# Optimization experiments

Measured on AMD Instinct MI355X. Metric: run time of the kernel, lower is better.

Reference implementation:

```python
import jax, jax.numpy as jnp
import numpy as np

# Static config matching init_kwargs
COUT, CIN, K = 64, 64, 3
PAD = K // 2  # padding=1


def setup_inputs() -> dict:
    key = jax.random.key(0)
    k1, k2, k3 = jax.random.split(key, 3)
    B, H, W, FH, FW, SC = 2, 256, 256, 16, 16, 128
    hyper_params = COUT * CIN * K * K  # 36864
    x = jax.random.normal(k1, (B, CIN, H, W), jnp.float32)
    s = jax.random.normal(k2, (B, SC, FH, FW), jnp.float32)
    s2w = jax.random.normal(k3, (hyper_params, SC), jnp.float32) * 0.02
    return {"x": x, "s": s, "s2w": s2w}


def reference(x, s, s2w):
    """HyperPatchConv2d forward: per-patch dynamically generated 3x3 conv.

    x:   [b, c, h, w]   input feature map
    s:   [b, sc, fh, fw] hypernetwork signal (one vector per patch)
    s2w: [P, sc]         signal2weights 1x1 conv (P = out*cin*k*k)
    """
    b, c, h, w = x.shape
    fh, fw = s.shape[-2:]
    ph, pw = h // fh, w // fw          # patch size
    kh, kw = ph + 2 * PAD, pw + 2 * PAD  # unfold window (patch + halo)

    # signal2weights: 1x1 conv -> per-patch flattened conv weight
    wflat = jnp.einsum('pc,bcfg->bfgp', s2w, s)            # [b,fh,fw,P]
    Wdyn = wflat.reshape(b, fh, fw, COUT, CIN, K, K)        # per-patch conv kernels

    # reflect-pad then unfold into overlapping (kh,kw) patches, stride (ph,pw)
    xp = jnp.pad(x, ((0, 0), (0, 0), (PAD, PAD), (PAD, PAD)), mode='reflect')
    idx_h = (jnp.arange(fh) * ph)[:, None] + jnp.arange(kh)[None, :]  # [fh,kh]
    idx_w = (jnp.arange(fw) * pw)[:, None] + jnp.arange(kw)[None, :]  # [fw,kw]
    patches = xp[:, :, idx_h][:, :, :, :, idx_w]            # [b,c,fh,kh,fw,kw]

    # extract KxK sliding windows inside each patch (valid conv, stride 1)
    wi = jnp.arange(ph)[:, None] + jnp.arange(K)[None, :]   # [ph,K]
    wj = jnp.arange(pw)[:, None] + jnp.arange(K)[None, :]   # [pw,K]
    win = patches[:, :, :, wi]                              # [b,c,fh,ph,K,fw,kw]
    win = win[:, :, :, :, :, :, wj]                         # [b,c,fh,ph,K,fw,pw,K]
    win = win.transpose(0, 2, 5, 1, 3, 4, 6, 7)             # [b,fh,fw,c,ph,K,pw,K]

    # per-patch dynamic conv
    out = jnp.einsum('bfgocij,bfgcpiqj->bfgopq', Wdyn, win)  # [b,fh,fw,o,ph,pw]

    # fold: non-overlapping reassembly (stride == patch size)
    return out.transpose(0, 3, 1, 4, 2, 5).reshape(b, COUT, h, w)
```

## Files before the change

kernel.cpp:

```cpp
#include <hip/hip_runtime.h>
#include <hip/hip_bf16.h>


#define C_OUT 64
#define C_IN  64
#define P_TOTAL 36864
#define N_PATCH 512
#define WSTR 72
#define GPLANE 1032

typedef __bf16 bf16x8 __attribute__((ext_vector_type(8)));
typedef float  f32x4  __attribute__((ext_vector_type(4)));

__device__ __forceinline__ unsigned short f2bf(float f) {
  unsigned int u = __float_as_uint(f);
  u += 0x7fffu + ((u >> 16) & 1u);
  return (unsigned short)(u >> 16);
}

__global__ __launch_bounds__(256) void prep_s2w(
    const float* __restrict__ s2w, unsigned short* __restrict__ A0) {
  const int gid = blockIdx.x * 256 + threadIdx.x;
  const int m = gid >> 5;
  const int k4 = (gid & 31) * 4;
  const int co = m / 576;
  const int r = m - co * 576;
  const int tap = r >> 6;
  const int ci = r & 63;
  const int p = co * 576 + ci * 9 + tap;
  const float4 v = *(const float4*)(s2w + (size_t)p * 128 + k4);
  ushort4 o;
  o.x = f2bf(v.x); o.y = f2bf(v.y); o.z = f2bf(v.z); o.w = f2bf(v.w);
  *(ushort4*)(A0 + (size_t)m * 128 + k4) = o;
}

__global__ __launch_bounds__(256) void prep_s(
    const float* __restrict__ s, unsigned short* __restrict__ sT) {
  const int bb = blockIdx.x;
  const int fg = threadIdx.x;
  unsigned short* dst = sT + ((size_t)bb * 256 + fg) * 128;
  for (int k = 0; k < 128; k += 2) {
    const float a = s[(size_t)(bb * 128 + k) * 256 + fg];
    const float b = s[(size_t)(bb * 128 + k + 1) * 256 + fg];
    const unsigned int u = (unsigned int)f2bf(a) | ((unsigned int)f2bf(b) << 16);
    *(unsigned int*)(dst + k) = u;
  }
}

__global__ __launch_bounds__(256) void prep_x(
    const float* __restrict__ x, unsigned short* __restrict__ xT) {
  __shared__ unsigned short lds[256 * 68];
  const int bb = blockIdx.x >> 8;
  const int row = blockIdx.x & 255;
  const int t = threadIdx.x;
  const float* src = x + ((size_t)bb * 64) * 65536 + row * 256 + t;
  #pragma unroll 8
  for (int ci = 0; ci < 64; ++ci)
    lds[t * 68 + ci] = f2bf(src[(size_t)ci * 65536]);
  __syncthreads();
  unsigned short* dst = xT + ((size_t)(bb * 65536 + row * 256 + t)) * 64;
  #pragma unroll
  for (int k8 = 0; k8 < 8; ++k8) {
    const uint2 u0 = *(const uint2*)&lds[t * 68 + k8 * 8];
    const uint2 u1 = *(const uint2*)&lds[t * 68 + k8 * 8 + 4];
    *(uint4*)(dst + k8 * 8) = make_uint4(u0.x, u0.y, u1.x, u1.y);
  }
}

__global__ __launch_bounds__(256) void wgen_kernel(
    const unsigned short* __restrict__ A0,
    const unsigned short* __restrict__ sT,
    unsigned short* __restrict__ wout)
{
  __shared__ unsigned short As[16 * GPLANE];
  __shared__ unsigned short Bs[16 * GPLANE];
  const int tid = threadIdx.x;
  const int m0 = blockIdx.x * 128;
  const int n0 = blockIdx.y * 128;

  #pragma unroll
  for (int i = 0; i < 8; ++i) {
    const int chunk = i * 256 + tid;
    const int row = chunk >> 4;
    const int g = chunk & 15;
    *(uint4*)&As[g * GPLANE + row * 8] = *(const uint4*)(A0 + ((size_t)(m0 + row)) * 128 + g * 8);
    *(uint4*)&Bs[g * GPLANE + row * 8] = *(const uint4*)(sT + ((size_t)(n0 + row)) * 128 + g * 8);
  }
  __syncthreads();

  const int wave = tid >> 6;
  const int lane = tid & 63;
  const int col = lane & 15;
  const int quad = lane >> 4;

  f32x4 acc[2][8] = {};
  #pragma unroll
  for (int ks = 0; ks < 4; ++ks) {
    const int g = ks * 4 + quad;
    bf16x8 afr[2], bfr[8];
    #pragma unroll
    for (int mti = 0; mti < 2; ++mti)
      afr[mti] = *(const bf16x8*)&As[g * GPLANE + ((wave * 2 + mti) * 16 + col) * 8];
    #pragma unroll
    for (int nt = 0; nt < 8; ++nt)
      bfr[nt] = *(const bf16x8*)&Bs[g * GPLANE + (nt * 16 + col) * 8];
    #pragma unroll
    for (int mti = 0; mti < 2; ++mti)
      #pragma unroll
      for (int nt = 0; nt < 8; ++nt)
        acc[mti][nt] = __builtin_amdgcn_mfma_f32_16x16x32_bf16(afr[mti], bfr[nt], acc[mti][nt], 0, 0, 0);
  }

  #pragma unroll
  for (int mti = 0; mti < 2; ++mti) {
    const int mbase = m0 + (wave * 2 + mti) * 16 + quad * 4;
    const int co = mbase / 576;
    const int rm = mbase - co * 576;
    const int tap = rm >> 6;
    const int ci = rm & 63;
    const size_t fragoff =
        ((size_t)((tap * 2 + (ci >> 5)) * 4 + (co >> 4)) * 64 + (co & 15) + 16 * ((ci >> 3) & 3)) * 8
        + (ci & 7);
    #pragma unroll
    for (int nt = 0; nt < 8; ++nt) {
      const int patch = n0 + nt * 16 + col;
      ushort4 o;
      o.x = f2bf(acc[mti][nt][0]); o.y = f2bf(acc[mti][nt][1]);
      o.z = f2bf(acc[mti][nt][2]); o.w = f2bf(acc[mti][nt][3]);
      *(ushort4*)(wout + (size_t)patch * P_TOTAL + fragoff) = o;
    }
  }
}

__global__ __launch_bounds__(256) void conv_kernel(
    const unsigned short* __restrict__ xT,
    const unsigned short* __restrict__ wfrag,
    float* __restrict__ out)
{
  __shared__ unsigned short win[324 * WSTR];
  const int tid = threadIdx.x;
  const int patch = blockIdx.x;
  const int bb = patch >> 8;
  const int fg = patch & 255;
  const int f = fg >> 4, g = fg & 15;
  const int row0 = f * 16, col0 = g * 16;

  for (int chunk = tid; chunk < 2592; chunk += 256) {
    const int cell = chunk >> 3;
    const int j = chunk & 7;
    const int r = cell / 18;
    const int c = cell - r * 18;
    int rr = row0 + r - 1; rr = rr < 0 ? -rr : (rr > 255 ? 510 - rr : rr);
    int cc = col0 + c - 1; cc = cc < 0 ? -cc : (cc > 255 ? 510 - cc : cc);
    *(uint4*)&win[cell * WSTR + j * 8] =
        *(const uint4*)(xT + ((size_t)((bb << 16) + (rr << 8) + cc)) * 64 + j * 8);
  }
  __syncthreads();

  const int wave = tid >> 6;
  const int lane = tid & 63;
  const int t = lane & 15;
  const int quad = lane >> 4;

  f32x4 acc[4][4] = {};
  const bf16x8* wb = (const bf16x8*)(wfrag + (size_t)patch * P_TOTAL);

  for (int tap = 0; tap < 9; ++tap) {
    const int ti = tap / 3;
    const int tj = tap - ti * 3;
    bf16x8 afr[2][4];
    #pragma unroll
    for (int ks = 0; ks < 2; ++ks)
      #pragma unroll
      for (int mt = 0; mt < 4; ++mt)
        afr[ks][mt] = wb[((tap * 2 + ks) * 4 + mt) * 64 + lane];

    #pragma unroll
    for (int nt = 0; nt < 4; ++nt) {
      const int r = wave * 4 + nt + ti;
      const int c = t + tj;
      const int base = (r * 18 + c) * WSTR + quad * 8;
      #pragma unroll
      for (int ks = 0; ks < 2; ++ks) {
        const bf16x8 bfr = *(const bf16x8*)&win[base + ks * 32];
        #pragma unroll
        for (int mt = 0; mt < 4; ++mt)
          acc[mt][nt] = __builtin_amdgcn_mfma_f32_16x16x32_bf16(afr[ks][mt], bfr, acc[mt][nt], 0, 0, 0);
      }
    }
  }

  #pragma unroll
  for (int mt = 0; mt < 4; ++mt) {
    #pragma unroll
    for (int nt = 0; nt < 4; ++nt) {
      const int p = row0 + wave * 4 + nt;
      #pragma unroll
      for (int reg = 0; reg < 4; ++reg) {
        const int co = mt * 16 + quad * 4 + reg;
        out[(((size_t)bb * C_OUT + co) << 16) + ((size_t)p << 8) + col0 + t] = acc[mt][nt][reg];
      }
    }
  }
}

extern "C" void kernel_launch(void* const* d_in, const int* in_sizes, int n_in,
                              void* d_out, int out_size, void* d_ws, size_t ws_size,
                              hipStream_t stream) {
  const float* x   = (const float*)d_in[0];
  const float* s   = (const float*)d_in[1];
  const float* s2w = (const float*)d_in[2];
  float* out = (float*)d_out;

  char* ws = (char*)d_ws;
  unsigned short* wbuf = (unsigned short*)(ws);
  unsigned short* A0   = (unsigned short*)(ws + 37748736);
  unsigned short* sT   = (unsigned short*)(ws + 47185920);
  unsigned short* xT   = (unsigned short*)(ws + 47316992);

  prep_s2w<<<4608, 256, 0, stream>>>(s2w, A0);
  prep_s<<<2, 256, 0, stream>>>(s, sT);
  prep_x<<<512, 256, 0, stream>>>(x, xT);
  wgen_kernel<<<dim3(288, 4), 256, 0, stream>>>(A0, sT, wbuf);
  conv_kernel<<<N_PATCH, 256, 0, stream>>>(xT, wbuf, out);
}
```

Measured before the change: 156.2 us.

## Fuse s2w conversion into wgen, stage output via LDS, widen conv blocks

The separate prep_s2w kernel is removed. wgen now reads fp32 s2w directly and converts it to bf16 while permuting rows straight into the conv fragment order, so the M dimension already matches the fragment layout. The GEMM result is transposed through LDS and written to global memory as coalesced 16-byte rows instead of scattered 8-byte stores. conv_kernel moves to 512 threads, each wave handling 2 rows instead of 4, which raises parallelism per patch at the cost of more redundant weight-fragment loads across waves.

```diff
diff --git a/kernel.cpp b/kernel.cpp
--- a/kernel.cpp
+++ b/kernel.cpp
@@ -8,6 +8,7 @@
 #define N_PATCH 512
 #define WSTR 72
 #define GPLANE 1032
+#define CSTR 136
 
 typedef __bf16 bf16x8 __attribute__((ext_vector_type(8)));
 typedef float  f32x4  __attribute__((ext_vector_type(4)));
@@ -16,22 +17,6 @@
   unsigned int u = __float_as_uint(f);
   u += 0x7fffu + ((u >> 16) & 1u);
   return (unsigned short)(u >> 16);
-}
-
-__global__ __launch_bounds__(256) void prep_s2w(
-    const float* __restrict__ s2w, unsigned short* __restrict__ A0) {
-  const int gid = blockIdx.x * 256 + threadIdx.x;
-  const int m = gid >> 5;
-  const int k4 = (gid & 31) * 4;
-  const int co = m / 576;
-  const int r = m - co * 576;
-  const int tap = r >> 6;
-  const int ci = r & 63;
-  const int p = co * 576 + ci * 9 + tap;
-  const float4 v = *(const float4*)(s2w + (size_t)p * 128 + k4);
-  ushort4 o;
-  o.x = f2bf(v.x); o.y = f2bf(v.y); o.z = f2bf(v.z); o.w = f2bf(v.w);
-  *(ushort4*)(A0 + (size_t)m * 128 + k4) = o;
 }
 
 __global__ __launch_bounds__(256) void prep_s(
@@ -68,22 +53,48 @@
 }
 
 __global__ __launch_bounds__(256) void wgen_kernel(
-    const unsigned short* __restrict__ A0,
+    const float* __restrict__ s2w,
     const unsigned short* __restrict__ sT,
     unsigned short* __restrict__ wout)
 {
-  __shared__ unsigned short As[16 * GPLANE];
-  __shared__ unsigned short Bs[16 * GPLANE];
+  __shared__ unsigned short smem[2 * 16 * GPLANE];
+  unsigned short* As = smem;
+  unsigned short* Bs = smem + 16 * GPLANE;
   const int tid = threadIdx.x;
   const int m0 = blockIdx.x * 128;
   const int n0 = blockIdx.y * 128;
+
+  const int fragidx = m0 >> 9;
+  const int tap = fragidx >> 3;
+  const int ksH = (fragidx >> 2) & 1;
+  const int mtH = fragidx & 3;
 
   #pragma unroll
   for (int i = 0; i < 8; ++i) {
     const int chunk = i * 256 + tid;
     const int row = chunk >> 4;
     const int g = chunk & 15;
-    *(uint4*)&As[g * GPLANE + row * 8] = *(const uint4*)(A0 + ((size_t)(m0 + row)) * 128 + g * 8);
+    const int m = m0 + row;
+    const int j = m & 7;
+    const int lane6 = (m >> 3) & 63;
+    const int co = mtH * 16 + (lane6 & 15);
+    const int ci = ksH * 32 + (lane6 >> 4) * 8 + j;
+    const int p = co * 576 + ci * 9 + tap;
+    const float* src = s2w + (size_t)p * 128 + g * 8;
+    const float4 v0 = *(const float4*)src;
+    const float4 v1 = *(const float4*)(src + 4);
+    uint4 o;
+    o.x = (unsigned int)f2bf(v0.x) | ((unsigned int)f2bf(v0.y) << 16);
+    o.y = (unsigned int)f2bf(v0.z) | ((unsigned int)f2bf(v0.w) << 16);
+    o.z = (unsigned int)f2bf(v1.x) | ((unsigned int)f2bf(v1.y) << 16);
+    o.w = (unsigned int)f2bf(v1.z) | ((unsigned int)f2bf(v1.w) << 16);
+    *(uint4*)&As[g * GPLANE + row * 8] = o;
+  }
+  #pragma unroll
+  for (int i = 0; i < 8; ++i) {
+    const int chunk = i * 256 + tid;
+    const int row = chunk >> 4;
+    const int g = chunk & 15;
     *(uint4*)&Bs[g * GPLANE + row * 8] = *(const uint4*)(sT + ((size_t)(n0 + row)) * 128 + g * 8);
   }
   __syncthreads();
@@ -111,28 +122,32 @@
         acc[mti][nt] = __builtin_amdgcn_mfma_f32_16x16x32_bf16(afr[mti], bfr[nt], acc[mti][nt], 0, 0, 0);
   }
 
+  __syncthreads();
+  unsigned short* Ct = smem;
   #pragma unroll
   for (int mti = 0; mti < 2; ++mti) {
-    const int mbase = m0 + (wave * 2 + mti) * 16 + quad * 4;
-    const int co = mbase / 576;
-    const int rm = mbase - co * 576;
-    const int tap = rm >> 6;
-    const int ci = rm & 63;
-    const size_t fragoff =
-        ((size_t)((tap * 2 + (ci >> 5)) * 4 + (co >> 4)) * 64 + (co & 15) + 16 * ((ci >> 3) & 3)) * 8
-        + (ci & 7);
+    const int mloc = (wave * 2 + mti) * 16 + quad * 4;
     #pragma unroll
     for (int nt = 0; nt < 8; ++nt) {
-      const int patch = n0 + nt * 16 + col;
+      const int pl = nt * 16 + col;
       ushort4 o;
       o.x = f2bf(acc[mti][nt][0]); o.y = f2bf(acc[mti][nt][1]);
       o.z = f2bf(acc[mti][nt][2]); o.w = f2bf(acc[mti][nt][3]);
-      *(ushort4*)(wout + (size_t)patch * P_TOTAL + fragoff) = o;
+      *(ushort4*)&Ct[pl * CSTR + mloc] = o;
     }
   }
-}
-
-__global__ __launch_bounds__(256) void conv_kernel(
+  __syncthreads();
+  #pragma unroll
+  for (int i = 0; i < 8; ++i) {
+    const int chunk = i * 256 + tid;
+    const int pl = chunk >> 4;
+    const int ii = chunk & 15;
+    const uint4 v = *(const uint4*)&Ct[pl * CSTR + ii * 8];
+    *(uint4*)(wout + (size_t)(n0 + pl) * P_TOTAL + m0 + ii * 8) = v;
+  }
+}
+
+__global__ __launch_bounds__(512) void conv_kernel(
     const unsigned short* __restrict__ xT,
     const unsigned short* __restrict__ wfrag,
     float* __restrict__ out)
@@ -145,7 +160,7 @@
   const int f = fg >> 4, g = fg & 15;
   const int row0 = f * 16, col0 = g * 16;
 
-  for (int chunk = tid; chunk < 2592; chunk += 256) {
+  for (int chunk = tid; chunk < 2592; chunk += 512) {
     const int cell = chunk >> 3;
     const int j = chunk & 7;
     const int r = cell / 18;
@@ -162,7 +177,7 @@
   const int t = lane & 15;
   const int quad = lane >> 4;
 
-  f32x4 acc[4][4] = {};
+  f32x4 acc[4][2] = {};
   const bf16x8* wb = (const bf16x8*)(wfrag + (size_t)patch * P_TOTAL);
 
   for (int tap = 0; tap < 9; ++tap) {
@@ -176,8 +191,8 @@
         afr[ks][mt] = wb[((tap * 2 + ks) * 4 + mt) * 64 + lane];
 
     #pragma unroll
-    for (int nt = 0; nt < 4; ++nt) {
-      const int r = wave * 4 + nt + ti;
+    for (int nt = 0; nt < 2; ++nt) {
+      const int r = wave * 2 + nt + ti;
       const int c = t + tj;
       const int base = (r * 18 + c) * WSTR + quad * 8;
       #pragma unroll
@@ -193,8 +208,8 @@
   #pragma unroll
   for (int mt = 0; mt < 4; ++mt) {
     #pragma unroll
-    for (int nt = 0; nt < 4; ++nt) {
-      const int p = row0 + wave * 4 + nt;
+    for (int nt = 0; nt < 2; ++nt) {
+      const int p = row0 + wave * 2 + nt;
       #pragma unroll
       for (int reg = 0; reg < 4; ++reg) {
         const int co = mt * 16 + quad * 4 + reg;
@@ -214,13 +229,11 @@
 
   char* ws = (char*)d_ws;
   unsigned short* wbuf = (unsigned short*)(ws);
-  unsigned short* A0   = (unsigned short*)(ws + 37748736);
-  unsigned short* sT   = (unsigned short*)(ws + 47185920);
-  unsigned short* xT   = (unsigned short*)(ws + 47316992);
-
-  prep_s2w<<<4608, 256, 0, stream>>>(s2w, A0);
+  unsigned short* sT   = (unsigned short*)(ws + 37748736);
+  unsigned short* xT   = (unsigned short*)(ws + 37879808);
+
   prep_s<<<2, 256, 0, stream>>>(s, sT);
   prep_x<<<512, 256, 0, stream>>>(x, xT);
-  wgen_kernel<<<dim3(288, 4), 256, 0, stream>>>(A0, sT, wbuf);
-  conv_kernel<<<N_PATCH, 256, 0, stream>>>(xT, wbuf, out);
-}
+  wgen_kernel<<<dim3(288, 4), 256, 0, stream>>>(s2w, sT, wbuf);
+  conv_kernel<<<N_PATCH, 512, 0, stream>>>(xT, wbuf, out);
+}
```

After: 139.7 us. -10.6%, faster.
